# Optimization experiments

Hardware: AMD Instinct MI355X
Metric: run time of the kernel (lower is better)

The kernel has to match this reference:

```python
import jax, jax.numpy as jnp
import numpy as np

N = 50000
E = 1600000
DIM = 128
RC = 5.0
DEPTH = 3


def setup_inputs() -> dict:
    key = jax.random.key(0)
    kv, ke, ks, kd, kw, kb, krs, ksig = jax.random.split(key, 8)
    v = jax.random.normal(kv, (N, DIM), dtype=jnp.float32)
    # edge distances in [0, rc]
    e = jax.random.uniform(ke, (E, 1), dtype=jnp.float32) * RC
    src = jax.random.randint(ks, (E,), 0, N, dtype=jnp.int32)
    dst = jax.random.randint(kd, (E,), 0, N, dtype=jnp.int32)
    # learned params: A = nn.Linear(dim, dim); rs, sigma = torch.rand(1)
    A_w = jax.random.normal(kw, (DIM, DIM), dtype=jnp.float32) / np.sqrt(DIM)
    A_b = jax.random.normal(kb, (DIM,), dtype=jnp.float32) * 0.01
    rs = jax.random.uniform(krs, (1,), dtype=jnp.float32)
    sigma = jax.random.uniform(ksig, (1,), dtype=jnp.float32)
    return {"v": v, "e": e, "src": src, "dst": dst,
            "A_w": A_w, "A_b": A_b, "rs": rs, "sigma": sigma}


def _edge_envelope(r, rs, sigma):
    # exp(-(r-rs)^2/sigma^2) * 0.5 * cos(pi*r/rc) * (r < rc)
    gauss = jnp.exp(-jnp.square(r - rs) / jnp.square(sigma))
    cutoff = 0.5 * jnp.cos(np.pi * r / RC) * (r < RC).astype(r.dtype)
    return gauss * cutoff


def reference(v, e, src, dst, A_w, A_b, rs, sigma):
    f = _edge_envelope(e, rs, sigma)  # [E, 1]
    cur = v
    for _ in range(DEPTH):
        msg = f * cur[src]  # gather src node feats, weight by edge envelope: [E, DIM]
        svf = jax.ops.segment_sum(msg, dst, num_segments=N)  # scatter-sum to dst: [N, DIM]
        cur = jax.nn.relu((svf + v) @ A_w.T + A_b)  # linear + relu, skip from original v
    return cur
```

## Files before the change

kernel.cpp:

```cpp
#include <hip/hip_runtime.h>
#include <math.h>

#define N_NODES 50000
#define N_PAD   50048
#define N_EDGES 1600000
#define DIM     128
#define RCUT    5.0f
#define NGROUP  (N_PAD / 64)
#define NB_PRE  512
#define CH_PRE  (N_EDGES / NB_PRE)
#define NB_CONV 6250
#define NB_WPREP 8
#define NB_SUB  8
#define B_SUB   (NB_PRE / NB_SUB)
#define XPAD    136

typedef __attribute__((ext_vector_type(8))) __bf16 bf16x8;
typedef __attribute__((ext_vector_type(4))) float  f32x4;

__device__ __forceinline__ float bf_lo(unsigned int u) { return __uint_as_float(u << 16); }
__device__ __forceinline__ float bf_hi(unsigned int u) { return __uint_as_float(u & 0xffff0000u); }
__device__ __forceinline__ unsigned short f2bf(float x) {
    unsigned int u = __float_as_uint(x);
    u += 0x7fffu + ((u >> 16) & 1u);
    return (unsigned short)(u >> 16);
}

__global__ __launch_bounds__(256) void preA_kernel(
        const float* __restrict__ v, unsigned short* __restrict__ vb,
        const float* __restrict__ Aw, uint4* __restrict__ wfrag,
        const int* __restrict__ dst, int* __restrict__ partial) {
    int b = blockIdx.x;
    if (b < NB_CONV) {
        int i = b * 256 + threadIdx.x;
        float4 x = ((const float4*)v)[i];
        uint2 o;
        o.x = (unsigned)f2bf(x.x) | ((unsigned)f2bf(x.y) << 16);
        o.y = (unsigned)f2bf(x.z) | ((unsigned)f2bf(x.w) << 16);
        ((uint2*)vb)[i] = o;
    } else if (b < NB_CONV + NB_WPREP) {
        int t = (b - NB_CONV) * 256 + threadIdx.x;
        int lane = t & 63, nt = (t >> 6) & 7, kk = t >> 9;
        int n  = nt * 16 + (lane & 15);
        int k0 = kk * 32 + (lane >> 4) * 8;
        unsigned short h[8];
        #pragma unroll
        for (int i = 0; i < 8; ++i) h[i] = f2bf(Aw[n * DIM + k0 + i]);
        uint4 o;
        o.x = h[0] | ((unsigned)h[1] << 16); o.y = h[2] | ((unsigned)h[3] << 16);
        o.z = h[4] | ((unsigned)h[5] << 16); o.w = h[6] | ((unsigned)h[7] << 16);
        wfrag[t] = o;
    } else {
        __shared__ int h[NGROUP];
        int cb = b - NB_CONV - NB_WPREP, tid = threadIdx.x;
        for (int g = tid; g < NGROUP; g += 256) h[g] = 0;
        __syncthreads();
        int beg = cb * CH_PRE, end = beg + CH_PRE;
        for (int i = beg + tid; i < end; i += 256)
            atomicAdd(&h[dst[i] >> 6], 1);
        __syncthreads();
        for (int g = tid; g < NGROUP; g += 256) partial[cb * NGROUP + g] = h[g];
    }
}

__global__ __launch_bounds__(256) void ktot2_kernel(const int* __restrict__ partial,
                                                    int* __restrict__ partial2) {
    int gb = blockIdx.x & 3, bb = blockIdx.x >> 2;
    int g = gb * 256 + threadIdx.x;
    if (g >= NGROUP) return;
    int s = 0;
    int b0 = bb * B_SUB;
    for (int b = b0; b < b0 + B_SUB; ++b) s += partial[b * NGROUP + g];
    partial2[bb * NGROUP + g] = s;
}

__global__ __launch_bounds__(256) void kscan_kernel(const int* __restrict__ partial2,
                                                    int* __restrict__ goff) {
    __shared__ int part[256];
    int tid = threadIdx.x;
    int i0 = tid * 4;
    int v[4]; int s = 0;
    #pragma unroll
    for (int k = 0; k < 4; ++k) {
        int i = i0 + k; int t = 0;
        if (i < NGROUP) {
            #pragma unroll
            for (int bb = 0; bb < NB_SUB; ++bb) t += partial2[bb * NGROUP + i];
        }
        v[k] = t; s += t;
    }
    part[tid] = s; __syncthreads();
    for (int d = 1; d < 256; d <<= 1) {
        int val = (tid >= d) ? part[tid - d] : 0;
        __syncthreads(); part[tid] += val; __syncthreads();
    }
    int run = (tid == 0) ? 0 : part[tid - 1];
    #pragma unroll
    for (int k = 0; k < 4; ++k) {
        int i = i0 + k;
        if (i < NGROUP) { goff[i] = run; run += v[k]; }
    }
    if (tid == 0) goff[NGROUP] = N_EDGES;
}

__global__ __launch_bounds__(256) void kbase2_kernel(const int* __restrict__ partial,
                                                     const int* __restrict__ partial2,
                                                     const int* __restrict__ goff,
                                                     int* __restrict__ pbase) {
    int gb = blockIdx.x & 3, bb = blockIdx.x >> 2;
    int g = gb * 256 + threadIdx.x;
    if (g >= NGROUP) return;
    int run = goff[g];
    for (int b2 = 0; b2 < bb; ++b2) run += partial2[b2 * NGROUP + g];
    int b0 = bb * B_SUB;
    for (int b = b0; b < b0 + B_SUB; ++b) {
        pbase[b * NGROUP + g] = run;
        run += partial[b * NGROUP + g];
    }
}

__global__ __launch_bounds__(512) void reorder_kernel(
        const float* __restrict__ e,
        const int*   __restrict__ src,
        const int*   __restrict__ dst,
        const float* __restrict__ rs,
        const float* __restrict__ sigma,
        const int*   __restrict__ pbase,
        int2* __restrict__ metaT) {
    __shared__ int base[NGROUP];
    __shared__ int cnt[NGROUP];
    int b = blockIdx.x, tid = threadIdx.x;
    for (int g = tid; g < NGROUP; g += 512) { base[g] = pbase[b * NGROUP + g]; cnt[g] = 0; }
    __syncthreads();
    float rsv = rs[0], sg = sigma[0];
    int beg = b * CH_PRE, end = beg + CH_PRE;
    for (int i = beg + tid; i < end; i += 512) {
        float r  = e[i];
        float d  = r - rsv;
        float gauss = expf(-(d * d) / (sg * sg));
        float cut   = 0.5f * cosf(r * (float)(M_PI / (double)RCUT));
        cut = (r < RCUT) ? cut : 0.0f;
        float fe = gauss * cut;
        int dn = dst[i];
        int g  = dn >> 6;
        int lr = atomicAdd(&cnt[g], 1);
        metaT[base[g] + lr] = make_int2(src[i] * (DIM * 2) | ((dn & 63) << 24),
                                        __float_as_int(fe));
    }
}

__global__ __launch_bounds__(256) void tagsort_kernel(
        const int2* __restrict__ metaT,
        const int*  __restrict__ goff,
        int2* __restrict__ meta,
        int*  __restrict__ off) {
    __shared__ int cnt[64], base[64], cur[64];
    int g = blockIdx.x, tid = threadIdx.x;
    int sbeg = goff[g], send = goff[g + 1];
    if (tid < 64) cnt[tid] = 0;
    __syncthreads();
    for (int i = sbeg + tid; i < send; i += 256)
        atomicAdd(&cnt[(metaT[i].x >> 24) & 63], 1);
    __syncthreads();
    if (tid == 0) {
        int run = 0;
        #pragma unroll
        for (int t = 0; t < 64; ++t) { base[t] = run; cur[t] = run; run += cnt[t]; }
    }
    __syncthreads();
    if (tid < 64) {
        int node = g * 64 + tid;
        if (node <= N_NODES) off[node] = sbeg + base[tid];
    }
    __syncthreads();
    for (int i = sbeg + tid; i < send; i += 256) {
        int2 m = metaT[i];
        int tag = (m.x >> 24) & 63;
        int lr = atomicAdd(&cur[tag], 1);
        meta[sbeg + lr] = make_int2(m.x & 0x00FFFFFF, m.y);
    }
}

#define EDGE2(mx, mf, rr)                                        \
    do {                                                         \
        float ff = __int_as_float(mf);                           \
        a0 = fmaf(ff, bf_lo(rr), a0);                            \
        a1 = fmaf(ff, bf_hi(rr), a1);                            \
    } while (0)

__global__ __launch_bounds__(512, 6) void layer_kernel(
        const unsigned short* __restrict__ cur,
        const unsigned short* __restrict__ vb,
        const int2*  __restrict__ meta,
        const int*   __restrict__ off,
        const uint4* __restrict__ wfrag,
        const float* __restrict__ bias,
        unsigned short* __restrict__ out_bf,
        float* __restrict__ out_f,
        int last) {
    __shared__ unsigned short xlds[64 * XPAD];
    int tid  = threadIdx.x;
    int wv   = tid >> 6, lane = tid & 63;
    int g    = blockIdx.x;
    int n0   = g * 64 + wv * 8;

    int offidx = n0 + ((lane < 9) ? lane : 8);
    if (offidx > N_NODES) offidx = N_NODES;
    int myoff = off[offidx];

    const char* basec = (const char*)cur + lane * 4;

    #pragma unroll 1
    for (int q = 0; q < 8; ++q) {
        int nl = wv * 8 + q;
        int n  = n0 + q;
        float a0 = 0.f, a1 = 0.f;
        if (n < N_NODES) {
            unsigned vv = *(const unsigned*)((const char*)vb + (size_t)n * (DIM * 2) + lane * 4);
            a0 = bf_lo(vv); a1 = bf_hi(vv);
            int beg = __builtin_amdgcn_readlane(myoff, q);
            int end = __builtin_amdgcn_readlane(myoff, q + 1);
            int c = beg;
            if ((c & 1) && c < end) {
                int2 m = meta[c];
                unsigned rr = *(const unsigned*)(basec + (unsigned)m.x);
                EDGE2(m.x, m.y, rr);
                ++c;
            }
            for (; c + 16 <= end; c += 16) {
                int4 m0 = *(const int4*)(meta + c);
                int4 m1 = *(const int4*)(meta + c + 2);
                int4 m2 = *(const int4*)(meta + c + 4);
                int4 m3 = *(const int4*)(meta + c + 6);
                int4 m4 = *(const int4*)(meta + c + 8);
                int4 m5 = *(const int4*)(meta + c + 10);
                int4 m6 = *(const int4*)(meta + c + 12);
                int4 m7 = *(const int4*)(meta + c + 14);
                unsigned r0  = *(const unsigned*)(basec + (unsigned)m0.x);
                unsigned r1  = *(const unsigned*)(basec + (unsigned)m0.z);
                unsigned r2  = *(const unsigned*)(basec + (unsigned)m1.x);
                unsigned r3  = *(const unsigned*)(basec + (unsigned)m1.z);
                unsigned r4  = *(const unsigned*)(basec + (unsigned)m2.x);
                unsigned r5  = *(const unsigned*)(basec + (unsigned)m2.z);
                unsigned r6  = *(const unsigned*)(basec + (unsigned)m3.x);
                unsigned r7  = *(const unsigned*)(basec + (unsigned)m3.z);
                unsigned r8  = *(const unsigned*)(basec + (unsigned)m4.x);
                unsigned r9  = *(const unsigned*)(basec + (unsigned)m4.z);
                unsigned r10 = *(const unsigned*)(basec + (unsigned)m5.x);
                unsigned r11 = *(const unsigned*)(basec + (unsigned)m5.z);
                unsigned r12 = *(const unsigned*)(basec + (unsigned)m6.x);
                unsigned r13 = *(const unsigned*)(basec + (unsigned)m6.z);
                unsigned r14 = *(const unsigned*)(basec + (unsigned)m7.x);
                unsigned r15 = *(const unsigned*)(basec + (unsigned)m7.z);
                EDGE2(m0.x, m0.y, r0);  EDGE2(m0.z, m0.w, r1);
                EDGE2(m1.x, m1.y, r2);  EDGE2(m1.z, m1.w, r3);
                EDGE2(m2.x, m2.y, r4);  EDGE2(m2.z, m2.w, r5);
                EDGE2(m3.x, m3.y, r6);  EDGE2(m3.z, m3.w, r7);
                EDGE2(m4.x, m4.y, r8);  EDGE2(m4.z, m4.w, r9);
                EDGE2(m5.x, m5.y, r10); EDGE2(m5.z, m5.w, r11);
                EDGE2(m6.x, m6.y, r12); EDGE2(m6.z, m6.w, r13);
                EDGE2(m7.x, m7.y, r14); EDGE2(m7.z, m7.w, r15);
            }
            if (c + 8 <= end) {
                int4 m0 = *(const int4*)(meta + c);
                int4 m1 = *(const int4*)(meta + c + 2);
                int4 m2 = *(const int4*)(meta + c + 4);
                int4 m3 = *(const int4*)(meta + c + 6);
                unsigned r0 = *(const unsigned*)(basec + (unsigned)m0.x);
                unsigned r1 = *(const unsigned*)(basec + (unsigned)m0.z);
                unsigned r2 = *(const unsigned*)(basec + (unsigned)m1.x);
                unsigned r3 = *(const unsigned*)(basec + (unsigned)m1.z);
                unsigned r4 = *(const unsigned*)(basec + (unsigned)m2.x);
                unsigned r5 = *(const unsigned*)(basec + (unsigned)m2.z);
                unsigned r6 = *(const unsigned*)(basec + (unsigned)m3.x);
                unsigned r7 = *(const unsigned*)(basec + (unsigned)m3.z);
                EDGE2(m0.x, m0.y, r0); EDGE2(m0.z, m0.w, r1);
                EDGE2(m1.x, m1.y, r2); EDGE2(m1.z, m1.w, r3);
                EDGE2(m2.x, m2.y, r4); EDGE2(m2.z, m2.w, r5);
                EDGE2(m3.x, m3.y, r6); EDGE2(m3.z, m3.w, r7);
                c += 8;
            }
            for (; c < end; ++c) {
                int2 m = meta[c];
                unsigned rr = *(const unsigned*)(basec + (unsigned)m.x);
                EDGE2(m.x, m.y, rr);
            }
        }
        *(unsigned*)(xlds + nl * XPAD + lane * 2) =
            (unsigned)f2bf(a0) | ((unsigned)f2bf(a1) << 16);
    }
    __syncthreads();

    int quad = lane >> 4, l16 = lane & 15;
    int rb = wv >> 1, nh = wv & 1;
    f32x4 acc[4];
    #pragma unroll
    for (int j = 0; j < 4; ++j) acc[j] = (f32x4){0.f, 0.f, 0.f, 0.f};

    const unsigned short* xp = xlds + (rb * 16 + l16) * XPAD + quad * 8;
    #pragma unroll
    for (int kk = 0; kk < 4; ++kk) {
        bf16x8 af = *(const bf16x8*)(xp + kk * 32);
        #pragma unroll
        for (int j = 0; j < 4; ++j) {
            uint4 w = wfrag[(kk * 8 + nh * 4 + j) * 64 + lane];
            bf16x8 bfr = __builtin_bit_cast(bf16x8, w);
            acc[j] = __builtin_amdgcn_mfma_f32_16x16x32_bf16(af, bfr, acc[j], 0, 0, 0);
        }
    }

    int orow0 = g * 64 + rb * 16 + quad * 4;
    #pragma unroll
    for (int j = 0; j < 4; ++j) {
        int col = (nh * 4 + j) * 16 + l16;
        float b = bias[col];
        #pragma unroll
        for (int r = 0; r < 4; ++r) {
            int orow = orow0 + r;
            if (orow < N_NODES) {
                float val = fmaxf(acc[j][r] + b, 0.f);
                if (last) out_f[(size_t)orow * DIM + col] = val;
                else      out_bf[(size_t)orow * DIM + col] = f2bf(val);
            }
        }
    }
}

extern "C" void kernel_launch(void* const* d_in, const int* in_sizes, int n_in,
                              void* d_out, int out_size, void* d_ws, size_t ws_size,
                              hipStream_t stream) {
    const float* v     = (const float*)d_in[0];
    const float* e     = (const float*)d_in[1];
    const int*   src   = (const int*)  d_in[2];
    const int*   dst   = (const int*)  d_in[3];
    const float* Aw    = (const float*)d_in[4];
    const float* Ab    = (const float*)d_in[5];
    const float* rs    = (const float*)d_in[6];
    const float* sigma = (const float*)d_in[7];
    float* out = (float*)d_out;

    char* p = (char*)d_ws;
    int2*           meta  = (int2*)p;            p += (size_t)N_EDGES * 8;
    unsigned short* bufV  = (unsigned short*)p;  p += (size_t)N_PAD * DIM * 2;
    unsigned short* bufA  = (unsigned short*)p;  p += (size_t)N_PAD * DIM * 2;
    unsigned short* bufB  = (unsigned short*)p;  p += (size_t)N_PAD * DIM * 2;
    uint4*          wfrag = (uint4*)p;           p += 2048 * 16;
    int*            off   = (int*)p;             p += (size_t)(N_NODES + 1) * 4;
    int*            goff  = (int*)p;             p += (NGROUP + 2) * 4;
    int2* metaT    = (int2*)bufA;
    int*  partial  = (int*)bufB;
    int*  pbase    = partial + NB_PRE * NGROUP;
    int*  partial2 = pbase + NB_PRE * NGROUP;

    preA_kernel<<<NB_CONV + NB_WPREP + NB_PRE, 256, 0, stream>>>(
        v, bufV, Aw, wfrag, dst, partial);
    ktot2_kernel<<<4 * NB_SUB, 256, 0, stream>>>(partial, partial2);
    kscan_kernel<<<1, 256, 0, stream>>>(partial2, goff);
    kbase2_kernel<<<4 * NB_SUB, 256, 0, stream>>>(partial, partial2, goff, pbase);
    reorder_kernel<<<NB_PRE, 512, 0, stream>>>(e, src, dst, rs, sigma, pbase, metaT);
    tagsort_kernel<<<NGROUP, 256, 0, stream>>>(metaT, goff, meta, off);

    layer_kernel<<<NGROUP, 512, 0, stream>>>(bufV, bufV, meta, off, wfrag, Ab, bufB, nullptr, 0);
    layer_kernel<<<NGROUP, 512, 0, stream>>>(bufB, bufV, meta, off, wfrag, Ab, bufA, nullptr, 0);
    layer_kernel<<<NGROUP, 512, 0, stream>>>(bufA, bufV, meta, off, wfrag, Ab, nullptr, out, 1);
}
```

Before: 345.3 us.

## Build CSR with global atomics and shrink layer tiles to 16 nodes

Replaces the two-level group histogram, multi-kernel scan and tag-sort preprocessing with a per-node global-atomic histogram, a single-block node-level scan, and a reorder that places each edge directly with a global atomic cursor. This cuts several kernel launches and the intermediate metaT pass. The layer kernel now uses 128-thread blocks covering 16 nodes instead of 512-thread blocks covering 64, which gives more blocks and finer load balancing. In exchange the edge order within a node becomes nondeterministic, global atomics can contend, and the single-block scan over 50k nodes is serial work.

```diff
diff --git a/kernel.cpp b/kernel.cpp
--- a/kernel.cpp
+++ b/kernel.cpp
@@ -6,14 +6,14 @@
 #define N_EDGES 1600000
 #define DIM     128
 #define RCUT    5.0f
-#define NGROUP  (N_PAD / 64)
-#define NB_PRE  512
-#define CH_PRE  (N_EDGES / NB_PRE)
 #define NB_CONV 6250
 #define NB_WPREP 8
-#define NB_SUB  8
-#define B_SUB   (NB_PRE / NB_SUB)
+#define NB_HIST 512
+#define CH_HIST (N_EDGES / NB_HIST)
+#define NB_RE   512
+#define CH_RE   (N_EDGES / NB_RE)
 #define XPAD    136
+#define NTILE   (N_PAD / 16)
 
 typedef __attribute__((ext_vector_type(8))) __bf16 bf16x8;
 typedef __attribute__((ext_vector_type(4))) float  f32x4;
@@ -26,10 +26,10 @@
     return (unsigned short)(u >> 16);
 }
 
-__global__ __launch_bounds__(256) void preA_kernel(
+__global__ __launch_bounds__(256) void pre_kernel(
         const float* __restrict__ v, unsigned short* __restrict__ vb,
         const float* __restrict__ Aw, uint4* __restrict__ wfrag,
-        const int* __restrict__ dst, int* __restrict__ partial) {
+        const int* __restrict__ dst, int* __restrict__ hist) {
     int b = blockIdx.x;
     if (b < NB_CONV) {
         int i = b * 256 + threadIdx.x;
@@ -51,72 +51,36 @@
         o.z = h[4] | ((unsigned)h[5] << 16); o.w = h[6] | ((unsigned)h[7] << 16);
         wfrag[t] = o;
     } else {
-        __shared__ int h[NGROUP];
-        int cb = b - NB_CONV - NB_WPREP, tid = threadIdx.x;
-        for (int g = tid; g < NGROUP; g += 256) h[g] = 0;
-        __syncthreads();
-        int beg = cb * CH_PRE, end = beg + CH_PRE;
-        for (int i = beg + tid; i < end; i += 256)
-            atomicAdd(&h[dst[i] >> 6], 1);
-        __syncthreads();
-        for (int g = tid; g < NGROUP; g += 256) partial[cb * NGROUP + g] = h[g];
-    }
-}
-
-__global__ __launch_bounds__(256) void ktot2_kernel(const int* __restrict__ partial,
-                                                    int* __restrict__ partial2) {
-    int gb = blockIdx.x & 3, bb = blockIdx.x >> 2;
-    int g = gb * 256 + threadIdx.x;
-    if (g >= NGROUP) return;
+        int cb = b - NB_CONV - NB_WPREP;
+        int beg = cb * CH_HIST, end = beg + CH_HIST;
+        for (int i = beg + threadIdx.x; i < end; i += 256)
+            atomicAdd(&hist[dst[i]], 1);
+    }
+}
+
+__global__ __launch_bounds__(1024) void kscan_node_kernel(
+        const int* __restrict__ hist,
+        int* __restrict__ off, int* __restrict__ ncur) {
+    __shared__ int part[1024];
+    int tid = threadIdx.x;
+    const int CHK = (N_NODES + 1023) / 1024;
+    int i0 = tid * CHK;
     int s = 0;
-    int b0 = bb * B_SUB;
-    for (int b = b0; b < b0 + B_SUB; ++b) s += partial[b * NGROUP + g];
-    partial2[bb * NGROUP + g] = s;
-}
-
-__global__ __launch_bounds__(256) void kscan_kernel(const int* __restrict__ partial2,
-                                                    int* __restrict__ goff) {
-    __shared__ int part[256];
-    int tid = threadIdx.x;
-    int i0 = tid * 4;
-    int v[4]; int s = 0;
-    #pragma unroll
-    for (int k = 0; k < 4; ++k) {
-        int i = i0 + k; int t = 0;
-        if (i < NGROUP) {
-            #pragma unroll
-            for (int bb = 0; bb < NB_SUB; ++bb) t += partial2[bb * NGROUP + i];
-        }
-        v[k] = t; s += t;
+    for (int k = 0; k < CHK; ++k) {
+        int i = i0 + k;
+        if (i < N_NODES) s += hist[i];
     }
     part[tid] = s; __syncthreads();
-    for (int d = 1; d < 256; d <<= 1) {
+    for (int d = 1; d < 1024; d <<= 1) {
         int val = (tid >= d) ? part[tid - d] : 0;
         __syncthreads(); part[tid] += val; __syncthreads();
     }
     int run = (tid == 0) ? 0 : part[tid - 1];
-    #pragma unroll
-    for (int k = 0; k < 4; ++k) {
+    for (int k = 0; k < CHK; ++k) {
         int i = i0 + k;
-        if (i < NGROUP) { goff[i] = run; run += v[k]; }
-    }
-    if (tid == 0) goff[NGROUP] = N_EDGES;
-}
-
-__global__ __launch_bounds__(256) void kbase2_kernel(const int* __restrict__ partial,
-                                                     const int* __restrict__ partial2,
-                                                     const int* __restrict__ goff,
-                                                     int* __restrict__ pbase) {
-    int gb = blockIdx.x & 3, bb = blockIdx.x >> 2;
-    int g = gb * 256 + threadIdx.x;
-    if (g >= NGROUP) return;
-    int run = goff[g];
-    for (int b2 = 0; b2 < bb; ++b2) run += partial2[b2 * NGROUP + g];
-    int b0 = bb * B_SUB;
-    for (int b = b0; b < b0 + B_SUB; ++b) {
-        pbase[b * NGROUP + g] = run;
-        run += partial[b * NGROUP + g];
-    }
+        if (i < N_NODES) { off[i] = run; ncur[i] = run; run += hist[i]; }
+    }
+    if (tid == 0) off[N_NODES] = N_EDGES;
 }
 
 __global__ __launch_bounds__(512) void reorder_kernel(
@@ -125,15 +89,11 @@
         const int*   __restrict__ dst,
         const float* __restrict__ rs,
         const float* __restrict__ sigma,
-        const int*   __restrict__ pbase,
-        int2* __restrict__ metaT) {
-    __shared__ int base[NGROUP];
-    __shared__ int cnt[NGROUP];
+        int*  __restrict__ ncur,
+        int2* __restrict__ meta) {
     int b = blockIdx.x, tid = threadIdx.x;
-    for (int g = tid; g < NGROUP; g += 512) { base[g] = pbase[b * NGROUP + g]; cnt[g] = 0; }
-    __syncthreads();
     float rsv = rs[0], sg = sigma[0];
-    int beg = b * CH_PRE, end = beg + CH_PRE;
+    int beg = b * CH_RE, end = beg + CH_RE;
     for (int i = beg + tid; i < end; i += 512) {
         float r  = e[i];
         float d  = r - rsv;
@@ -142,42 +102,8 @@
         cut = (r < RCUT) ? cut : 0.0f;
         float fe = gauss * cut;
         int dn = dst[i];
-        int g  = dn >> 6;
-        int lr = atomicAdd(&cnt[g], 1);
-        metaT[base[g] + lr] = make_int2(src[i] * (DIM * 2) | ((dn & 63) << 24),
-                                        __float_as_int(fe));
-    }
-}
-
-__global__ __launch_bounds__(256) void tagsort_kernel(
-        const int2* __restrict__ metaT,
-        const int*  __restrict__ goff,
-        int2* __restrict__ meta,
-        int*  __restrict__ off) {
-    __shared__ int cnt[64], base[64], cur[64];
-    int g = blockIdx.x, tid = threadIdx.x;
-    int sbeg = goff[g], send = goff[g + 1];
-    if (tid < 64) cnt[tid] = 0;
-    __syncthreads();
-    for (int i = sbeg + tid; i < send; i += 256)
-        atomicAdd(&cnt[(metaT[i].x >> 24) & 63], 1);
-    __syncthreads();
-    if (tid == 0) {
-        int run = 0;
-        #pragma unroll
-        for (int t = 0; t < 64; ++t) { base[t] = run; cur[t] = run; run += cnt[t]; }
-    }
-    __syncthreads();
-    if (tid < 64) {
-        int node = g * 64 + tid;
-        if (node <= N_NODES) off[node] = sbeg + base[tid];
-    }
-    __syncthreads();
-    for (int i = sbeg + tid; i < send; i += 256) {
-        int2 m = metaT[i];
-        int tag = (m.x >> 24) & 63;
-        int lr = atomicAdd(&cur[tag], 1);
-        meta[sbeg + lr] = make_int2(m.x & 0x00FFFFFF, m.y);
+        int lr = atomicAdd(&ncur[dn], 1);
+        meta[lr] = make_int2(src[i] * (DIM * 2), __float_as_int(fe));
     }
 }
 
@@ -188,7 +114,77 @@
         a1 = fmaf(ff, bf_hi(rr), a1);                            \
     } while (0)
 
-__global__ __launch_bounds__(512, 6) void layer_kernel(
+__device__ __forceinline__ void gather_node(
+        const int2* __restrict__ meta, const char* basec,
+        int beg, int end, float& a0, float& a1) {
+    int c = beg;
+    if ((c & 1) && c < end) {
+        int2 m = meta[c];
+        unsigned rr = *(const unsigned*)(basec + (unsigned)m.x);
+        EDGE2(m.x, m.y, rr);
+        ++c;
+    }
+    for (; c + 16 <= end; c += 16) {
+        int4 m0 = *(const int4*)(meta + c);
+        int4 m1 = *(const int4*)(meta + c + 2);
+        int4 m2 = *(const int4*)(meta + c + 4);
+        int4 m3 = *(const int4*)(meta + c + 6);
+        int4 m4 = *(const int4*)(meta + c + 8);
+        int4 m5 = *(const int4*)(meta + c + 10);
+        int4 m6 = *(const int4*)(meta + c + 12);
+        int4 m7 = *(const int4*)(meta + c + 14);
+        unsigned r0  = *(const unsigned*)(basec + (unsigned)m0.x);
+        unsigned r1  = *(const unsigned*)(basec + (unsigned)m0.z);
+        unsigned r2  = *(const unsigned*)(basec + (unsigned)m1.x);
+        unsigned r3  = *(const unsigned*)(basec + (unsigned)m1.z);
+        unsigned r4  = *(const unsigned*)(basec + (unsigned)m2.x);
+        unsigned r5  = *(const unsigned*)(basec + (unsigned)m2.z);
+        unsigned r6  = *(const unsigned*)(basec + (unsigned)m3.x);
+        unsigned r7  = *(const unsigned*)(basec + (unsigned)m3.z);
+        unsigned r8  = *(const unsigned*)(basec + (unsigned)m4.x);
+        unsigned r9  = *(const unsigned*)(basec + (unsigned)m4.z);
+        unsigned r10 = *(const unsigned*)(basec + (unsigned)m5.x);
+        unsigned r11 = *(const unsigned*)(basec + (unsigned)m5.z);
+        unsigned r12 = *(const unsigned*)(basec + (unsigned)m6.x);
+        unsigned r13 = *(const unsigned*)(basec + (unsigned)m6.z);
+        unsigned r14 = *(const unsigned*)(basec + (unsigned)m7.x);
+        unsigned r15 = *(const unsigned*)(basec + (unsigned)m7.z);
+        EDGE2(m0.x, m0.y, r0);  EDGE2(m0.z, m0.w, r1);
+        EDGE2(m1.x, m1.y, r2);  EDGE2(m1.z, m1.w, r3);
+        EDGE2(m2.x, m2.y, r4);  EDGE2(m2.z, m2.w, r5);
+        EDGE2(m3.x, m3.y, r6);  EDGE2(m3.z, m3.w, r7);
+        EDGE2(m4.x, m4.y, r8);  EDGE2(m4.z, m4.w, r9);
+        EDGE2(m5.x, m5.y, r10); EDGE2(m5.z, m5.w, r11);
+        EDGE2(m6.x, m6.y, r12); EDGE2(m6.z, m6.w, r13);
+        EDGE2(m7.x, m7.y, r14); EDGE2(m7.z, m7.w, r15);
+    }
+    if (c + 8 <= end) {
+        int4 m0 = *(const int4*)(meta + c);
+        int4 m1 = *(const int4*)(meta + c + 2);
+        int4 m2 = *(const int4*)(meta + c + 4);
+        int4 m3 = *(const int4*)(meta + c + 6);
+        unsigned r0 = *(const unsigned*)(basec + (unsigned)m0.x);
+        unsigned r1 = *(const unsigned*)(basec + (unsigned)m0.z);
+        unsigned r2 = *(const unsigned*)(basec + (unsigned)m1.x);
+        unsigned r3 = *(const unsigned*)(basec + (unsigned)m1.z);
+        unsigned r4 = *(const unsigned*)(basec + (unsigned)m2.x);
+        unsigned r5 = *(const unsigned*)(basec + (unsigned)m2.z);
+        unsigned r6 = *(const unsigned*)(basec + (unsigned)m3.x);
+        unsigned r7 = *(const unsigned*)(basec + (unsigned)m3.z);
+        EDGE2(m0.x, m0.y, r0); EDGE2(m0.z, m0.w, r1);
+        EDGE2(m1.x, m1.y, r2); EDGE2(m1.z, m1.w, r3);
+        EDGE2(m2.x, m2.y, r4); EDGE2(m2.z, m2.w, r5);
+        EDGE2(m3.x, m3.y, r6); EDGE2(m3.z, m3.w, r7);
+        c += 8;
+    }
+    for (; c < end; ++c) {
+        int2 m = meta[c];
+        unsigned rr = *(const unsigned*)(basec + (unsigned)m.x);
+        EDGE2(m.x, m.y, rr);
+    }
+}
+
+__global__ __launch_bounds__(128, 8) void layer_kernel(
         const unsigned short* __restrict__ cur,
         const unsigned short* __restrict__ vb,
         const int2*  __restrict__ meta,
@@ -198,16 +194,15 @@
         unsigned short* __restrict__ out_bf,
         float* __restrict__ out_f,
         int last) {
-    __shared__ unsigned short xlds[64 * XPAD];
-    int tid  = threadIdx.x;
-    int wv   = tid >> 6, lane = tid & 63;
-    int g    = blockIdx.x;
-    int n0   = g * 64 + wv * 8;
+    __shared__ unsigned short xlds[16 * XPAD];
+    int tid = threadIdx.x;
+    int wv  = tid >> 6, lane = tid & 63;
+    int tile = blockIdx.x;
+    int n0  = tile * 16 + wv * 8;
 
     int offidx = n0 + ((lane < 9) ? lane : 8);
     if (offidx > N_NODES) offidx = N_NODES;
     int myoff = off[offidx];
-
     const char* basec = (const char*)cur + lane * 4;
 
     #pragma unroll 1
@@ -220,71 +215,7 @@
             a0 = bf_lo(vv); a1 = bf_hi(vv);
             int beg = __builtin_amdgcn_readlane(myoff, q);
             int end = __builtin_amdgcn_readlane(myoff, q + 1);
-            int c = beg;
-            if ((c & 1) && c < end) {
-                int2 m = meta[c];
-                unsigned rr = *(const unsigned*)(basec + (unsigned)m.x);
-                EDGE2(m.x, m.y, rr);
-                ++c;
-            }
-            for (; c + 16 <= end; c += 16) {
-                int4 m0 = *(const int4*)(meta + c);
-                int4 m1 = *(const int4*)(meta + c + 2);
-                int4 m2 = *(const int4*)(meta + c + 4);
-                int4 m3 = *(const int4*)(meta + c + 6);
-                int4 m4 = *(const int4*)(meta + c + 8);
-                int4 m5 = *(const int4*)(meta + c + 10);
-                int4 m6 = *(const int4*)(meta + c + 12);
-                int4 m7 = *(const int4*)(meta + c + 14);
-                unsigned r0  = *(const unsigned*)(basec + (unsigned)m0.x);
-                unsigned r1  = *(const unsigned*)(basec + (unsigned)m0.z);
-                unsigned r2  = *(const unsigned*)(basec + (unsigned)m1.x);
-                unsigned r3  = *(const unsigned*)(basec + (unsigned)m1.z);
-                unsigned r4  = *(const unsigned*)(basec + (unsigned)m2.x);
-                unsigned r5  = *(const unsigned*)(basec + (unsigned)m2.z);
-                unsigned r6  = *(const unsigned*)(basec + (unsigned)m3.x);
-                unsigned r7  = *(const unsigned*)(basec + (unsigned)m3.z);
-                unsigned r8  = *(const unsigned*)(basec + (unsigned)m4.x);
-                unsigned r9  = *(const unsigned*)(basec + (unsigned)m4.z);
-                unsigned r10 = *(const unsigned*)(basec + (unsigned)m5.x);
-                unsigned r11 = *(const unsigned*)(basec + (unsigned)m5.z);
-                unsigned r12 = *(const unsigned*)(basec + (unsigned)m6.x);
-                unsigned r13 = *(const unsigned*)(basec + (unsigned)m6.z);
-                unsigned r14 = *(const unsigned*)(basec + (unsigned)m7.x);
-                unsigned r15 = *(const unsigned*)(basec + (unsigned)m7.z);
-                EDGE2(m0.x, m0.y, r0);  EDGE2(m0.z, m0.w, r1);
-                EDGE2(m1.x, m1.y, r2);  EDGE2(m1.z, m1.w, r3);
-                EDGE2(m2.x, m2.y, r4);  EDGE2(m2.z, m2.w, r5);
-                EDGE2(m3.x, m3.y, r6);  EDGE2(m3.z, m3.w, r7);
-                EDGE2(m4.x, m4.y, r8);  EDGE2(m4.z, m4.w, r9);
-                EDGE2(m5.x, m5.y, r10); EDGE2(m5.z, m5.w, r11);
-                EDGE2(m6.x, m6.y, r12); EDGE2(m6.z, m6.w, r13);
-                EDGE2(m7.x, m7.y, r14); EDGE2(m7.z, m7.w, r15);
-            }
-            if (c + 8 <= end) {
-                int4 m0 = *(const int4*)(meta + c);
-                int4 m1 = *(const int4*)(meta + c + 2);
-                int4 m2 = *(const int4*)(meta + c + 4);
-                int4 m3 = *(const int4*)(meta + c + 6);
-                unsigned r0 = *(const unsigned*)(basec + (unsigned)m0.x);
-                unsigned r1 = *(const unsigned*)(basec + (unsigned)m0.z);
-                unsigned r2 = *(const unsigned*)(basec + (unsigned)m1.x);
-                unsigned r3 = *(const unsigned*)(basec + (unsigned)m1.z);
-                unsigned r4 = *(const unsigned*)(basec + (unsigned)m2.x);
-                unsigned r5 = *(const unsigned*)(basec + (unsigned)m2.z);
-                unsigned r6 = *(const unsigned*)(basec + (unsigned)m3.x);
-                unsigned r7 = *(const unsigned*)(basec + (unsigned)m3.z);
-                EDGE2(m0.x, m0.y, r0); EDGE2(m0.z, m0.w, r1);
-                EDGE2(m1.x, m1.y, r2); EDGE2(m1.z, m1.w, r3);
-                EDGE2(m2.x, m2.y, r4); EDGE2(m2.z, m2.w, r5);
-                EDGE2(m3.x, m3.y, r6); EDGE2(m3.z, m3.w, r7);
-                c += 8;
-            }
-            for (; c < end; ++c) {
-                int2 m = meta[c];
-                unsigned rr = *(const unsigned*)(basec + (unsigned)m.x);
-                EDGE2(m.x, m.y, rr);
-            }
+            gather_node(meta, basec, beg, end, a0, a1);
         }
         *(unsigned*)(xlds + nl * XPAD + lane * 2) =
             (unsigned)f2bf(a0) | ((unsigned)f2bf(a1) << 16);
@@ -292,27 +223,26 @@
     __syncthreads();
 
     int quad = lane >> 4, l16 = lane & 15;
-    int rb = wv >> 1, nh = wv & 1;
     f32x4 acc[4];
     #pragma unroll
     for (int j = 0; j < 4; ++j) acc[j] = (f32x4){0.f, 0.f, 0.f, 0.f};
 
-    const unsigned short* xp = xlds + (rb * 16 + l16) * XPAD + quad * 8;
+    const unsigned short* xp = xlds + l16 * XPAD + quad * 8;
     #pragma unroll
     for (int kk = 0; kk < 4; ++kk) {
         bf16x8 af = *(const bf16x8*)(xp + kk * 32);
         #pragma unroll
         for (int j = 0; j < 4; ++j) {
-            uint4 w = wfrag[(kk * 8 + nh * 4 + j) * 64 + lane];
+            uint4 w = wfrag[(kk * 8 + wv * 4 + j) * 64 + lane];
             bf16x8 bfr = __builtin_bit_cast(bf16x8, w);
             acc[j] = __builtin_amdgcn_mfma_f32_16x16x32_bf16(af, bfr, acc[j], 0, 0, 0);
         }
     }
 
-    int orow0 = g * 64 + rb * 16 + quad * 4;
+    int orow0 = tile * 16 + quad * 4;
     #pragma unroll
     for (int j = 0; j < 4; ++j) {
-        int col = (nh * 4 + j) * 16 + l16;
+        int col = (wv * 4 + j) * 16 + l16;
         float b = bias[col];
         #pragma unroll
         for (int r = 0; r < 4; ++r) {
@@ -345,22 +275,20 @@
     unsigned short* bufA  = (unsigned short*)p;  p += (size_t)N_PAD * DIM * 2;
     unsigned short* bufB  = (unsigned short*)p;  p += (size_t)N_PAD * DIM * 2;
     uint4*          wfrag = (uint4*)p;           p += 2048 * 16;
-    int*            off   = (int*)p;             p += (size_t)(N_NODES + 1) * 4;
-    int*            goff  = (int*)p;             p += (NGROUP + 2) * 4;
-    int2* metaT    = (int2*)bufA;
-    int*  partial  = (int*)bufB;
-    int*  pbase    = partial + NB_PRE * NGROUP;
-    int*  partial2 = pbase + NB_PRE * NGROUP;
-
-    preA_kernel<<<NB_CONV + NB_WPREP + NB_PRE, 256, 0, stream>>>(
-        v, bufV, Aw, wfrag, dst, partial);
-    ktot2_kernel<<<4 * NB_SUB, 256, 0, stream>>>(partial, partial2);
-    kscan_kernel<<<1, 256, 0, stream>>>(partial2, goff);
-    kbase2_kernel<<<4 * NB_SUB, 256, 0, stream>>>(partial, partial2, goff, pbase);
-    reorder_kernel<<<NB_PRE, 512, 0, stream>>>(e, src, dst, rs, sigma, pbase, metaT);
-    tagsort_kernel<<<NGROUP, 256, 0, stream>>>(metaT, goff, meta, off);
-
-    layer_kernel<<<NGROUP, 512, 0, stream>>>(bufV, bufV, meta, off, wfrag, Ab, bufB, nullptr, 0);
-    layer_kernel<<<NGROUP, 512, 0, stream>>>(bufB, bufV, meta, off, wfrag, Ab, bufA, nullptr, 0);
-    layer_kernel<<<NGROUP, 512, 0, stream>>>(bufA, bufV, meta, off, wfrag, Ab, nullptr, out, 1);
-}
+    int*            off   = (int*)p;             p += (size_t)(N_NODES + 2) * 4;
+    int*            ncur  = (int*)p;             p += (size_t)N_NODES * 4;
+    int*            hist  = (int*)p;             p += (size_t)N_NODES * 4;
+
+    hipMemsetAsync(hist, 0, (size_t)N_NODES * 4, stream);
+    pre_kernel<<<NB_CONV + NB_WPREP + NB_HIST, 256, 0, stream>>>(
+        v, bufV, Aw, wfrag, dst, hist);
+    kscan_node_kernel<<<1, 1024, 0, stream>>>(hist, off, ncur);
+    reorder_kernel<<<NB_RE, 512, 0, stream>>>(e, src, dst, rs, sigma, ncur, meta);
+
+    layer_kernel<<<NTILE, 128, 0, stream>>>(
+        bufV, bufV, meta, off, wfrag, Ab, bufB, nullptr, 0);
+    layer_kernel<<<NTILE, 128, 0, stream>>>(
+        bufB, bufV, meta, off, wfrag, Ab, bufA, nullptr, 0);
+    layer_kernel<<<NTILE, 128, 0, stream>>>(
+        bufA, bufV, meta, off, wfrag, Ab, nullptr, out, 1);
+}
```

Result: slower. 589.3 us (+70.7%).
